# Kernel optimization log

Hardware: AMD Instinct MI355X
Metric: run time of the kernel (lower is better)

## Reference

```python
import jax, jax.numpy as jnp
import numpy as np

# Static config matching init_kwargs / forward constants
H = 12          # num_heads
D = 64          # head_dim
SW = 64         # kv_cache_sliding_window (frames)
SF = 8          # kv_cache_scale_frames
NUM_REG = 4     # num_register_tokens -> camera_idx=0, scale_idx=5
SPECIAL_END = NUM_REG + 2  # camera..scale inclusive slice = tokens [0:6)


def setup_inputs() -> dict:
    key = jax.random.key(0)
    ks = jax.random.split(key, 9)
    B, N, C = 1, 576, 768
    T = 192  # tokens per frame; num_frame_per_block = N // T = 3
    inp = {
        'x': jax.random.normal(ks[0], (B, N, C), jnp.float32),
        'qkv_w': jax.random.normal(ks[1], (3 * C, C), jnp.float32) * (C ** -0.5),
        'qkv_b': jax.random.normal(ks[2], (3 * C,), jnp.float32) * 0.02,
        'proj_w': jax.random.normal(ks[3], (C, C), jnp.float32) * (C ** -0.5),
        'proj_b': jax.random.normal(ks[4], (C,), jnp.float32) * 0.02,
        'k_cache': jax.random.normal(ks[5], (B, H, SW + SF, T, D), jnp.float32),
        'v_cache': jax.random.normal(ks[6], (B, H, SW + SF, T, D), jnp.float32),
        'k_special': jax.random.normal(ks[7], (B, H, 12, SPECIAL_END, D), jnp.float32),
        'v_special': jax.random.normal(ks[8], (B, H, 12, SPECIAL_END, D), jnp.float32),
    }
    return inp


def reference(x, qkv_w, qkv_b, proj_w, proj_b, k_cache, v_cache, k_special, v_special):
    B, N, C = x.shape
    T = k_cache.shape[3]           # tokens per frame
    nfb = N // T                   # num_frame_per_block (inferred, as in torch code)

    # qkv projection: (B,N,3C) -> (3,B,H,N,D)
    qkv = (x @ qkv_w.T + qkv_b).reshape(B, N, 3, H, D).transpose(2, 0, 3, 1, 4)
    q, k, v = qkv[0], qkv[1], qkv[2]   # each (B,H,N,D); q_norm/k_norm = Identity

    # Append new block frames to the cache
    k_cache = jnp.concatenate([k_cache, k.reshape(B, H, nfb, T, D)], axis=2)
    v_cache = jnp.concatenate([v_cache, v.reshape(B, H, nfb, T, D)], axis=2)

    # Sliding-window eviction (shapes chosen so this branch always fires)
    F = k_cache.shape[2]
    evict_start, evict_end = SF, F - SW   # 8 .. 11
    # cross-frame special tokens: camera..scale (tokens 0:6) of evicted frames
    new_sk = k_cache[:, :, evict_start:evict_end, :SPECIAL_END, :]
    new_sv = v_cache[:, :, evict_start:evict_end, :SPECIAL_END, :]
    k_special = jnp.concatenate([k_special, new_sk], axis=2)
    v_special = jnp.concatenate([v_special, new_sv], axis=2)
    # keep scale frames + last sliding_window frames
    k_cache = jnp.concatenate([k_cache[:, :, :SF], k_cache[:, :, -SW:]], axis=2)
    v_cache = jnp.concatenate([v_cache[:, :, :SF], v_cache[:, :, -SW:]], axis=2)

    # Flatten frames -> tokens; prepend special tokens
    k_full = jnp.concatenate([k_special.reshape(B, H, -1, D),
                              k_cache.reshape(B, H, -1, D)], axis=2)
    v_full = jnp.concatenate([v_special.reshape(B, H, -1, D),
                              v_cache.reshape(B, H, -1, D)], axis=2)

    # SDPA (no mask, no dropout, default scale 1/sqrt(D))
    scale = 1.0 / jnp.sqrt(jnp.float32(D))
    scores = jnp.einsum('bhnd,bhmd->bhnm', q, k_full) * scale
    attn = jax.nn.softmax(scores, axis=-1)
    out = jnp.einsum('bhnm,bhmd->bhnd', attn, v_full)

    out = out.transpose(0, 2, 1, 3).reshape(B, N, H * D)
    return out @ proj_w.T + proj_b
```

## Files before the change

kernel.cpp:

```cpp
#include <hip/hip_runtime.h>
#include <hip/hip_bf16.h>

#define NH    12
#define HD    64
#define NT    576
#define CC    768
#define M_TOT 13914
#define MP    13952
#define NTIL  218
#define NEW0  13338

typedef short bf16x8 __attribute__((ext_vector_type(8)));
typedef float f32x4 __attribute__((ext_vector_type(4)));
typedef float f32x16 __attribute__((ext_vector_type(16)));

#define QSCALE 0.18033688011112042f

__device__ __forceinline__ unsigned pk2(float a, float b) {
  __hip_bfloat162 h = __float22bfloat162_rn(make_float2(a, b));
  return *(unsigned*)&h;
}

__global__ __launch_bounds__(256) void cvt_all(
    const float* __restrict__ x, const float* __restrict__ wsrc,
    const float* __restrict__ pw, __hip_bfloat16* __restrict__ xb,
    __hip_bfloat16* __restrict__ wb, __hip_bfloat16* __restrict__ wph,
    __hip_bfloat16* __restrict__ wpl) {
  const int nx8 = NT * CC / 8;
  const int nw8 = 3 * CC * CC / 8;
  const int npw8 = CC * CC / 8;
  int i = blockIdx.x * 256 + threadIdx.x;
  if (i < nx8 + nw8) {
    const float* src; __hip_bfloat16* dst; int j;
    if (i < nx8) { src = x; dst = xb; j = i; }
    else { j = i - nx8; src = wsrc; dst = wb; }
    const float4 a = ((const float4*)src)[2 * j];
    const float4 b = ((const float4*)src)[2 * j + 1];
    __hip_bfloat16 t[8];
    t[0] = __float2bfloat16(a.x); t[1] = __float2bfloat16(a.y);
    t[2] = __float2bfloat16(a.z); t[3] = __float2bfloat16(a.w);
    t[4] = __float2bfloat16(b.x); t[5] = __float2bfloat16(b.y);
    t[6] = __float2bfloat16(b.z); t[7] = __float2bfloat16(b.w);
    ((uint4*)dst)[j] = *(const uint4*)t;
  } else {
    const int j = i - nx8 - nw8;
    if (j >= npw8) return;
    float v[8];
    const float4 a = ((const float4*)pw)[2 * j];
    const float4 b = ((const float4*)pw)[2 * j + 1];
    v[0] = a.x; v[1] = a.y; v[2] = a.z; v[3] = a.w;
    v[4] = b.x; v[5] = b.y; v[6] = b.z; v[7] = b.w;
    __hip_bfloat16 th[8], tl[8];
#pragma unroll
    for (int e = 0; e < 8; ++e) {
      th[e] = __float2bfloat16(v[e]);
      tl[e] = __float2bfloat16(v[e] - __bfloat162float(th[e]));
    }
    ((uint4*)wph)[j] = *(const uint4*)th;
    ((uint4*)wpl)[j] = *(const uint4*)tl;
  }
}

__device__ __forceinline__ const float* kv_src_row(
    const float* __restrict__ cache, const float* __restrict__ special,
    int h, int m) {
  if (m < 72) return special + ((size_t)h * 72 + m) * HD;
  if (m < 90) {
    const int j = m - 72;
    return cache + (((size_t)h * 72 + 8 + j / 6) * 192 + (j % 6)) * HD;
  }
  if (m < 1626) return cache + ((size_t)h * 13824 + (m - 90)) * HD;
  return cache + ((size_t)h * 13824 + 2112 + (m - 1626)) * HD;
}

#define GEMM_BLKS 324
#define VT_BLKS   2616
#define KB_BLKS   10004

__global__ __launch_bounds__(256) void qkv_and_gather(
    const __hip_bfloat16* __restrict__ xb, const __hip_bfloat16* __restrict__ wb,
    const float* __restrict__ bias, __hip_bfloat16* __restrict__ Qb,
    __hip_bfloat16* __restrict__ Kf, __hip_bfloat16* __restrict__ Vt,
    const float* __restrict__ kc, const float* __restrict__ ksp,
    const float* __restrict__ vc, const float* __restrict__ vsp) {
  __shared__ float vsf[64][68];
  const int bx = blockIdx.x;
  const int tid = threadIdx.x;

  if (bx < GEMM_BLKS) {
    const int w = tid >> 6, l = tid & 63, l15 = l & 15, lg = l >> 4;
    const int n0 = (bx % 36) * 64;
    const int mw = (bx / 36) * 64 + w * 16;

    f32x4 acc[4];
#pragma unroll
    for (int nt = 0; nt < 4; ++nt) acc[nt] = (f32x4){0.f, 0.f, 0.f, 0.f};

    const __hip_bfloat16* arow = xb + (size_t)(mw + l15) * CC + 8 * lg;
#pragma unroll 4
    for (int k0 = 0; k0 < CC; k0 += 32) {
      const bf16x8 a = *(const bf16x8*)(arow + k0);
#pragma unroll
      for (int nt = 0; nt < 4; ++nt) {
        const bf16x8 b =
            *(const bf16x8*)(wb + (size_t)(n0 + nt * 16 + l15) * CC + k0 + 8 * lg);
        acc[nt] = __builtin_amdgcn_mfma_f32_16x16x32_bf16(a, b, acc[nt], 0, 0, 0);
      }
    }
#pragma unroll
    for (int nt = 0; nt < 4; ++nt) {
      const int c = n0 + nt * 16 + l15;
      const int which = c / CC;
      const int rem = c - which * CC;
      const int hh = rem >> 6;
      const int dd = rem & 63;
      const float bc = bias[c];
#pragma unroll
      for (int r = 0; r < 4; ++r) {
        const int m = mw + 4 * lg + r;
        const float v = acc[nt][r] + bc;
        if (which == 0) {
          Qb[((size_t)hh * NT + m) * HD + dd] = __float2bfloat16(v * QSCALE);
        } else if (which == 1) {
          Kf[((size_t)hh * MP + NEW0 + m) * HD + dd] = __float2bfloat16(v);
        } else {
          Vt[((size_t)hh * HD + dd) * MP + NEW0 + m] = __float2bfloat16(v);
        }
      }
    }
  } else if (bx < GEMM_BLKS + VT_BLKS) {
    const int tv = bx - GEMM_BLKS;
    const int m0 = (tv % 218) * 64;
    const int h = tv / 218;
    if (m0 >= NEW0) return;
#pragma unroll
    for (int p = 0; p < 4; ++p) {
      const int mr = m0 + p * 16 + (tid >> 4);
      const int c4 = (tid & 15) * 4;
      float4 v = make_float4(0.f, 0.f, 0.f, 0.f);
      if (mr < NEW0) v = *(const float4*)(kv_src_row(vc, vsp, h, mr) + c4);
      *(float4*)&vsf[p * 16 + (tid >> 4)][c4] = v;
    }
    __syncthreads();
#pragma unroll
    for (int e0 = 0; e0 < 2; ++e0) {
      const int e = tid + e0 * 256;
      const int d = e >> 3;
      const int ms = (e & 7) * 8;
      __hip_bfloat16 t[8];
#pragma unroll
      for (int j = 0; j < 8; ++j) t[j] = __float2bfloat16(vsf[ms + j][d]);
      __hip_bfloat16* dst = Vt + ((size_t)h * HD + d) * MP + m0 + ms;
      if (m0 + ms + 8 <= NEW0) {
        *(uint4*)dst = *(const uint4*)t;
      } else {
#pragma unroll
        for (int j = 0; j < 8; ++j)
          if (m0 + ms + j < NEW0) dst[j] = t[j];
      }
    }
  } else {
    const int idx = (bx - GEMM_BLKS - VT_BLKS) * 256 + tid;
    const int per_h = NEW0 * 16;
    if (idx >= NH * per_h) return;
    const int h = idx / per_h;
    const int r = idx - h * per_h;
    const int m = r >> 4;
    const int dq = (r & 15) << 2;
    const float4 v = *(const float4*)(kv_src_row(kc, ksp, h, m) + dq);
    __hip_bfloat162* dst = (__hip_bfloat162*)(Kf + ((size_t)h * MP + m) * HD + dq);
    __hip_bfloat162 a, b;
    a.x = __float2bfloat16(v.x); a.y = __float2bfloat16(v.y);
    b.x = __float2bfloat16(v.z); b.y = __float2bfloat16(v.w);
    dst[0] = a; dst[1] = b;
  }
}

template <int S>
__global__ __launch_bounds__(256, 4) void attn_partial(
    const __hip_bfloat16* __restrict__ Qb, const __hip_bfloat16* __restrict__ Kf,
    const __hip_bfloat16* __restrict__ Vt, float* __restrict__ Opart,
    float2* __restrict__ mlpart) {
  __shared__ __align__(16) char lds[32768];

  const int tid = threadIdx.x;
  const int w = tid >> 6, l = tid & 63;
  const int l31 = l & 31, hi = l >> 5;

  const int i = blockIdx.x;
  const int per_xcd = (5 * NH * S) / 8;
  const int work = (i & 7) * per_xcd + (i >> 3);
  const int qt = work % 5;
  const int hs = work / 5;
  const int h = hs % NH;
  const int strip = hs / NH;

  const int qrow = qt * 128 + w * 32 + l31;
  const int qrc = qrow < NT ? qrow : NT - 1;

  bf16x8 qreg[4];
  {
    const __hip_bfloat16* qp = Qb + ((size_t)h * NT + qrc) * HD + 8 * hi;
#pragma unroll
    for (int s4 = 0; s4 < 4; ++s4) qreg[s4] = *(const bf16x8*)(qp + 16 * s4);
  }

  f32x16 oacc0, oacc1;
#pragma unroll
  for (int r = 0; r < 16; ++r) { oacc0[r] = 0.f; oacc1[r] = 0.f; }
  float m_run = -1e30f, l_run = 0.f;

  const __hip_bfloat16* Kh = Kf + (size_t)h * MP * HD;
  const __hip_bfloat16* Vth = Vt + (size_t)h * HD * MP;

  const int srow0 = tid >> 3;
  const int srow1 = 32 + (tid >> 3);
  const int sp8 = (tid & 7) * 8;
  const unsigned soff0 =
      ((unsigned)((srow0 << 7) | ((tid & 7) << 4))) ^ ((srow0 & 7) << 4);
  const unsigned soff1 =
      ((unsigned)((srow1 << 7) | ((tid & 7) << 4))) ^ ((srow1 & 7) << 4);

  uint4 kd0, kd1, vd0, vd1;
  auto issue = [&](int t) {
    const int m0 = t * 64;
    kd0 = *(const uint4*)(Kh + (size_t)(m0 + srow0) * HD + sp8);
    kd1 = *(const uint4*)(Kh + (size_t)(m0 + srow1) * HD + sp8);
    vd0 = *(const uint4*)(Vth + (size_t)srow0 * MP + m0 + sp8);
    vd1 = *(const uint4*)(Vth + (size_t)srow1 * MP + m0 + sp8);
  };
  auto commit = [&](char* buf) {
    *(uint4*)(buf + soff0) = kd0;
    *(uint4*)(buf + soff1) = kd1;
    *(uint4*)(buf + 8192 + soff0) = vd0;
    *(uint4*)(buf + 8192 + soff1) = vd1;
  };

  issue(strip);
  commit(lds);
  __syncthreads();

  int cur = 0;
  for (int t = strip; t < NTIL; t += S) {
    const int tn = t + S;
    if (tn < NTIL) issue(tn);

    char* ksb = lds + (cur << 14);
    char* vtb = ksb + 8192;
    const int m0 = t * 64;

    f32x16 sc0, sc1;
#pragma unroll
    for (int r = 0; r < 16; ++r) { sc0[r] = 0.f; sc1[r] = 0.f; }
#pragma unroll
    for (int s4 = 0; s4 < 4; ++s4) {
      const int cb = 32 * s4 + 16 * hi;
      const unsigned o0 = ((unsigned)((l31 << 7) | cb)) ^ ((l31 & 7) << 4);
      const unsigned o1 = ((unsigned)(((l31 + 32) << 7) | cb)) ^ ((l31 & 7) << 4);
      const bf16x8 a0 = *(const bf16x8*)(ksb + o0);
      const bf16x8 a1 = *(const bf16x8*)(ksb + o1);
      sc0 = __builtin_amdgcn_mfma_f32_32x32x16_bf16(a0, qreg[s4], sc0, 0, 0, 0);
      sc1 = __builtin_amdgcn_mfma_f32_32x32x16_bf16(a1, qreg[s4], sc1, 0, 0, 0);
    }

    if (m0 + 64 > M_TOT) {
#pragma unroll
      for (int r = 0; r < 16; ++r) {
        const int base = (r & 3) + 8 * (r >> 2) + 4 * hi;
        if (m0 + base >= M_TOT) sc0[r] = -1e30f;
        if (m0 + 32 + base >= M_TOT) sc1[r] = -1e30f;
      }
    }

    float mt = sc0[0];
#pragma unroll
    for (int r = 1; r < 16; ++r) mt = fmaxf(mt, sc0[r]);
#pragma unroll
    for (int r = 0; r < 16; ++r) mt = fmaxf(mt, sc1[r]);
    mt = fmaxf(mt, __shfl_xor(mt, 32));

    if (__any(mt > m_run + 8.f)) {
      const float mn = fmaxf(m_run, mt);
      const float corr = exp2f(m_run - mn);
      m_run = mn;
      l_run *= corr;
#pragma unroll
      for (int r = 0; r < 16; ++r) { oacc0[r] *= corr; oacc1[r] *= corr; }
    }

    float psum = 0.f;
    unsigned W0[8], W1[8];
#pragma unroll
    for (int i2 = 0; i2 < 8; ++i2) {
      const float e0 = exp2f(sc0[2 * i2] - m_run);
      const float e1 = exp2f(sc0[2 * i2 + 1] - m_run);
      const float f0 = exp2f(sc1[2 * i2] - m_run);
      const float f1 = exp2f(sc1[2 * i2 + 1] - m_run);
      psum += (e0 + e1) + (f0 + f1);
      W0[i2] = pk2(e0, e1);
      W1[i2] = pk2(f0, f1);
    }
    psum += __shfl_xor(psum, 32);
    l_run += psum;

#pragma unroll
    for (int s4 = 0; s4 < 4; ++s4) {
      const int u = s4 & 1;
      const unsigned a0 = (s4 < 2) ? W0[4 * u + 0] : W1[4 * u + 0];
      const unsigned a1 = (s4 < 2) ? W0[4 * u + 1] : W1[4 * u + 1];
      const unsigned a2 = (s4 < 2) ? W0[4 * u + 2] : W1[4 * u + 2];
      const unsigned a3 = (s4 < 2) ? W0[4 * u + 3] : W1[4 * u + 3];
      const unsigned x0 = (unsigned)__shfl_xor((int)a0, 32);
      const unsigned x1 = (unsigned)__shfl_xor((int)a1, 32);
      const unsigned x2 = (unsigned)__shfl_xor((int)a2, 32);
      const unsigned x3 = (unsigned)__shfl_xor((int)a3, 32);
      union { unsigned u4[4]; bf16x8 v; } pa;
      pa.u4[0] = hi ? x2 : a0;
      pa.u4[1] = hi ? x3 : a1;
      pa.u4[2] = hi ? a2 : x0;
      pa.u4[3] = hi ? a3 : x1;
      const int cb = 32 * s4 + 16 * hi;
#pragma unroll
      for (int dh = 0; dh < 2; ++dh) {
        const int vr = 32 * dh + l31;
        const unsigned ov = ((unsigned)((vr << 7) | cb)) ^ ((vr & 7) << 4);
        const bf16x8 va = *(const bf16x8*)(vtb + ov);
        if (dh == 0)
          oacc0 = __builtin_amdgcn_mfma_f32_32x32x16_bf16(va, pa.v, oacc0, 0, 0, 0);
        else
          oacc1 = __builtin_amdgcn_mfma_f32_32x32x16_bf16(va, pa.v, oacc1, 0, 0, 0);
      }
    }

    if (tn < NTIL) commit(lds + ((cur ^ 1) << 14));
    __syncthreads();
    cur ^= 1;
  }

  if (qrow < NT) {
    float* Op = Opart + (((size_t)strip * NH + h) * NT + qrow) * HD;
#pragma unroll
    for (int g = 0; g < 4; ++g) {
      f32x4 o0 = {oacc0[4 * g], oacc0[4 * g + 1], oacc0[4 * g + 2], oacc0[4 * g + 3]};
      f32x4 o1 = {oacc1[4 * g], oacc1[4 * g + 1], oacc1[4 * g + 2], oacc1[4 * g + 3]};
      *(f32x4*)(Op + 8 * g + 4 * hi) = o0;
      *(f32x4*)(Op + 32 + 8 * g + 4 * hi) = o1;
    }
    if (hi == 0)
      mlpart[((size_t)strip * NH + h) * NT + qrow] = make_float2(m_run, l_run);
  }
}

template <int S>
__global__ __launch_bounds__(256) void attn_merge(
    const float* __restrict__ Opart, const float2* __restrict__ mlpart,
    __hip_bfloat16* __restrict__ Owh, __hip_bfloat16* __restrict__ Owl) {
  const int idx = blockIdx.x * 256 + threadIdx.x;
  if (idx >= NH * NT * HD) return;
  const int d = idx & 63;
  const int hn = idx >> 6;
  const int n = hn % NT;
  const int h = hn / NT;
  float M = -1e30f;
  float m[S], lv[S];
#pragma unroll
  for (int s = 0; s < S; ++s) {
    const float2 ml = mlpart[((size_t)s * NH + h) * NT + n];
    m[s] = ml.x; lv[s] = ml.y;
    M = fmaxf(M, m[s]);
  }
  float L = 0.f, O = 0.f;
#pragma unroll
  for (int s = 0; s < S; ++s) {
    const float e = exp2f(m[s] - M);
    L += lv[s] * e;
    O += Opart[(((size_t)s * NH + h) * NT + n) * HD + d] * e;
  }
  const float v = O / L;
  const __hip_bfloat16 hB = __float2bfloat16(v);
  const size_t o = (size_t)n * CC + h * HD + d;
  Owh[o] = hB;
  Owl[o] = __float2bfloat16(v - __bfloat162float(hB));
}

__global__ __launch_bounds__(256) void gemm_proj_mfma(
    const __hip_bfloat16* __restrict__ Ah, const __hip_bfloat16* __restrict__ Al,
    const __hip_bfloat16* __restrict__ Wh, const __hip_bfloat16* __restrict__ Wl,
    const float* __restrict__ bias, float* __restrict__ out_f) {
  const int tid = threadIdx.x;
  const int w = tid >> 6, l = tid & 63, l15 = l & 15, lg = l >> 4;
  const int n0 = blockIdx.x * 64;
  const int mw = blockIdx.y * 64 + w * 16;

  f32x4 acc[4];
#pragma unroll
  for (int nt = 0; nt < 4; ++nt) acc[nt] = (f32x4){0.f, 0.f, 0.f, 0.f};

  const __hip_bfloat16* ah = Ah + (size_t)(mw + l15) * CC + 8 * lg;
  const __hip_bfloat16* al = Al + (size_t)(mw + l15) * CC + 8 * lg;
#pragma unroll 2
  for (int k0 = 0; k0 < CC; k0 += 32) {
    const bf16x8 a0 = *(const bf16x8*)(ah + k0);
    const bf16x8 a1 = *(const bf16x8*)(al + k0);
#pragma unroll
    for (int nt = 0; nt < 4; ++nt) {
      const size_t wi = (size_t)(n0 + nt * 16 + l15) * CC + k0 + 8 * lg;
      const bf16x8 bh = *(const bf16x8*)(Wh + wi);
      const bf16x8 bl = *(const bf16x8*)(Wl + wi);
      acc[nt] = __builtin_amdgcn_mfma_f32_16x16x32_bf16(a0, bh, acc[nt], 0, 0, 0);
      acc[nt] = __builtin_amdgcn_mfma_f32_16x16x32_bf16(a0, bl, acc[nt], 0, 0, 0);
      acc[nt] = __builtin_amdgcn_mfma_f32_16x16x32_bf16(a1, bh, acc[nt], 0, 0, 0);
    }
  }
#pragma unroll
  for (int nt = 0; nt < 4; ++nt) {
    const int c = n0 + nt * 16 + l15;
    const float bc = bias[c];
#pragma unroll
    for (int r = 0; r < 4; ++r)
      out_f[(size_t)(mw + 4 * lg + r) * CC + c] = acc[nt][r] + bc;
  }
}

extern "C" void kernel_launch(void* const* d_in, const int* in_sizes, int n_in,
                              void* d_out, int out_size, void* d_ws,
                              size_t ws_size, hipStream_t stream) {
  const float* x       = (const float*)d_in[0];
  const float* qkv_w   = (const float*)d_in[1];
  const float* qkv_b   = (const float*)d_in[2];
  const float* proj_w  = (const float*)d_in[3];
  const float* proj_b  = (const float*)d_in[4];
  const float* k_cache = (const float*)d_in[5];
  const float* v_cache = (const float*)d_in[6];
  const float* k_specl = (const float*)d_in[7];
  const float* v_specl = (const float*)d_in[8];
  float* out = (float*)d_out;

  const size_t qb_bytes = (size_t)NH * NT * HD * 2;
  const size_t kv_bytes = (size_t)NH * MP * HD * 2;
  const size_t xb_bytes = (size_t)NT * CC * 2;
  const size_t wb_bytes = (size_t)3 * CC * CC * 2;
  const size_t pw_bytes = (size_t)CC * CC * 2;
  const size_t owh_bytes = (size_t)NT * CC * 2;

  auto need = [&](int S) -> size_t {
    const size_t op = (size_t)S * NH * NT * HD * 4;
    const size_t ml = (size_t)S * NH * NT * 8;
    const size_t opr = op > xb_bytes + wb_bytes ? op : xb_bytes + wb_bytes;
    return qb_bytes + 2 * kv_bytes + opr + ml + 2 * pw_bytes;
  };
  const int S = (need(16) <= ws_size) ? 16 : 8;
  const size_t op_bytes = (size_t)S * NH * NT * HD * 4;
  const size_t ml_bytes = (size_t)S * NH * NT * 8;
  const size_t opr = op_bytes > xb_bytes + wb_bytes ? op_bytes : xb_bytes + wb_bytes;

  char* ws = (char*)d_ws;
  __hip_bfloat16* Qb = (__hip_bfloat16*)ws;
  char* kf_region = ws + qb_bytes;
  __hip_bfloat16* Kf = (__hip_bfloat16*)kf_region;
  __hip_bfloat16* Vt = (__hip_bfloat16*)(kf_region + kv_bytes);
  char* opp = kf_region + 2 * kv_bytes;
  float* Opart = (float*)opp;
  __hip_bfloat16* xb = (__hip_bfloat16*)opp;
  __hip_bfloat16* wb = (__hip_bfloat16*)(opp + xb_bytes);
  float2* mlpart = (float2*)(opp + opr);
  __hip_bfloat16* wph = (__hip_bfloat16*)(opp + opr + ml_bytes);
  __hip_bfloat16* wpl = (__hip_bfloat16*)(opp + opr + ml_bytes + pw_bytes);
  __hip_bfloat16* Owh = (__hip_bfloat16*)kf_region;
  __hip_bfloat16* Owl = (__hip_bfloat16*)(kf_region + owh_bytes);

  cvt_all<<<dim3(1368), 256, 0, stream>>>(x, qkv_w, proj_w, xb, wb, wph, wpl);
  qkv_and_gather<<<dim3(GEMM_BLKS + VT_BLKS + KB_BLKS), 256, 0, stream>>>(
      xb, wb, qkv_b, Qb, Kf, Vt, k_cache, k_specl, v_cache, v_specl);
  if (S == 16) {
    attn_partial<16><<<dim3(5 * NH * 16), 256, 0, stream>>>(Qb, Kf, Vt, Opart, mlpart);
    attn_merge<16><<<dim3((NH * NT * HD + 255) / 256), 256, 0, stream>>>(
        Opart, mlpart, Owh, Owl);
  } else {
    attn_partial<8><<<dim3(5 * NH * 8), 256, 0, stream>>>(Qb, Kf, Vt, Opart, mlpart);
    attn_merge<8><<<dim3((NH * NT * HD + 255) / 256), 256, 0, stream>>>(
        Opart, mlpart, Owh, Owl);
  }
  gemm_proj_mfma<<<dim3(12, 9), 256, 0, stream>>>(Owh, Owl, wph, wpl, proj_b, out);
}
```

Baseline: 141.4 us.

## Fuse K-cache fp32-to-bf16 gather into attention kernel, drop double buffering

Removes the separate K gather and convert pass from the qkv kernel. The attention kernel now reads fp32 K rows straight from the cache and special-token buffers, converts them to bf16 in registers, and writes them into LDS. This avoids writing and re-reading a bf16 K copy, but each K tile is now read as fp32 by every query tile (5 times). The register-prefetch double buffer is replaced by a single-buffered load-sync-compute loop, and the projection GEMM uses 32-wide N tiles to launch twice as many blocks.

```diff
diff --git a/kernel.cpp b/kernel.cpp
--- a/kernel.cpp
+++ b/kernel.cpp
@@ -75,13 +75,11 @@
 
 #define GEMM_BLKS 324
 #define VT_BLKS   2616
-#define KB_BLKS   10004
 
 __global__ __launch_bounds__(256) void qkv_and_gather(
     const __hip_bfloat16* __restrict__ xb, const __hip_bfloat16* __restrict__ wb,
     const float* __restrict__ bias, __hip_bfloat16* __restrict__ Qb,
     __hip_bfloat16* __restrict__ Kf, __hip_bfloat16* __restrict__ Vt,
-    const float* __restrict__ kc, const float* __restrict__ ksp,
     const float* __restrict__ vc, const float* __restrict__ vsp) {
   __shared__ float vsf[64][68];
   const int bx = blockIdx.x;
@@ -128,7 +126,7 @@
         }
       }
     }
-  } else if (bx < GEMM_BLKS + VT_BLKS) {
+  } else {
     const int tv = bx - GEMM_BLKS;
     const int m0 = (tv % 218) * 64;
     const int h = tv / 218;
@@ -159,29 +157,18 @@
           if (m0 + ms + j < NEW0) dst[j] = t[j];
       }
     }
-  } else {
-    const int idx = (bx - GEMM_BLKS - VT_BLKS) * 256 + tid;
-    const int per_h = NEW0 * 16;
-    if (idx >= NH * per_h) return;
-    const int h = idx / per_h;
-    const int r = idx - h * per_h;
-    const int m = r >> 4;
-    const int dq = (r & 15) << 2;
-    const float4 v = *(const float4*)(kv_src_row(kc, ksp, h, m) + dq);
-    __hip_bfloat162* dst = (__hip_bfloat162*)(Kf + ((size_t)h * MP + m) * HD + dq);
-    __hip_bfloat162 a, b;
-    a.x = __float2bfloat16(v.x); a.y = __float2bfloat16(v.y);
-    b.x = __float2bfloat16(v.z); b.y = __float2bfloat16(v.w);
-    dst[0] = a; dst[1] = b;
   }
 }
 
 template <int S>
 __global__ __launch_bounds__(256, 4) void attn_partial(
     const __hip_bfloat16* __restrict__ Qb, const __hip_bfloat16* __restrict__ Kf,
-    const __hip_bfloat16* __restrict__ Vt, float* __restrict__ Opart,
+    const __hip_bfloat16* __restrict__ Vt, const float* __restrict__ kc,
+    const float* __restrict__ ksp, float* __restrict__ Opart,
     float2* __restrict__ mlpart) {
-  __shared__ __align__(16) char lds[32768];
+  __shared__ __align__(16) char lds[16384];
+  char* ksb = lds;
+  char* vtb = lds + 8192;
 
   const int tid = threadIdx.x;
   const int w = tid >> 6, l = tid & 63;
@@ -221,33 +208,28 @@
   const unsigned soff1 =
       ((unsigned)((srow1 << 7) | ((tid & 7) << 4))) ^ ((srow1 & 7) << 4);
 
-  uint4 kd0, kd1, vd0, vd1;
-  auto issue = [&](int t) {
+  for (int t = strip; t < NTIL; t += S) {
     const int m0 = t * 64;
-    kd0 = *(const uint4*)(Kh + (size_t)(m0 + srow0) * HD + sp8);
-    kd1 = *(const uint4*)(Kh + (size_t)(m0 + srow1) * HD + sp8);
-    vd0 = *(const uint4*)(Vth + (size_t)srow0 * MP + m0 + sp8);
-    vd1 = *(const uint4*)(Vth + (size_t)srow1 * MP + m0 + sp8);
-  };
-  auto commit = [&](char* buf) {
-    *(uint4*)(buf + soff0) = kd0;
-    *(uint4*)(buf + soff1) = kd1;
-    *(uint4*)(buf + 8192 + soff0) = vd0;
-    *(uint4*)(buf + 8192 + soff1) = vd1;
-  };
-
-  issue(strip);
-  commit(lds);
-  __syncthreads();
-
-  int cur = 0;
-  for (int t = strip; t < NTIL; t += S) {
-    const int tn = t + S;
-    if (tn < NTIL) issue(tn);
-
-    char* ksb = lds + (cur << 14);
-    char* vtb = ksb + 8192;
-    const int m0 = t * 64;
+#pragma unroll
+    for (int e = 0; e < 4; ++e) {
+      const int c = tid + 256 * e;
+      const int row = c >> 4, ci = c & 15;
+      const int m = m0 + row;
+      const unsigned off =
+          ((unsigned)((row << 7) | (ci << 3))) ^ ((unsigned)(row & 7) << 4);
+      uint2 w8;
+      if (m < NEW0) {
+        const float4 v = *(const float4*)(kv_src_row(kc, ksp, h, m) + 4 * ci);
+        w8.x = pk2(v.x, v.y);
+        w8.y = pk2(v.z, v.w);
+      } else {
+        w8 = *(const uint2*)(Kh + (size_t)m * HD + 4 * ci);
+      }
+      *(uint2*)(ksb + off) = w8;
+    }
+    *(uint4*)(vtb + soff0) = *(const uint4*)(Vth + (size_t)srow0 * MP + m0 + sp8);
+    *(uint4*)(vtb + soff1) = *(const uint4*)(Vth + (size_t)srow1 * MP + m0 + sp8);
+    __syncthreads();
 
     f32x16 sc0, sc1;
 #pragma unroll
@@ -331,10 +313,7 @@
           oacc1 = __builtin_amdgcn_mfma_f32_32x32x16_bf16(va, pa.v, oacc1, 0, 0, 0);
       }
     }
-
-    if (tn < NTIL) commit(lds + ((cur ^ 1) << 14));
     __syncthreads();
-    cur ^= 1;
   }
 
   if (qrow < NT) {
@@ -389,12 +368,12 @@
     const float* __restrict__ bias, float* __restrict__ out_f) {
   const int tid = threadIdx.x;
   const int w = tid >> 6, l = tid & 63, l15 = l & 15, lg = l >> 4;
-  const int n0 = blockIdx.x * 64;
+  const int n0 = blockIdx.x * 32;
   const int mw = blockIdx.y * 64 + w * 16;
 
-  f32x4 acc[4];
-#pragma unroll
-  for (int nt = 0; nt < 4; ++nt) acc[nt] = (f32x4){0.f, 0.f, 0.f, 0.f};
+  f32x4 acc[2];
+#pragma unroll
+  for (int nt = 0; nt < 2; ++nt) acc[nt] = (f32x4){0.f, 0.f, 0.f, 0.f};
 
   const __hip_bfloat16* ah = Ah + (size_t)(mw + l15) * CC + 8 * lg;
   const __hip_bfloat16* al = Al + (size_t)(mw + l15) * CC + 8 * lg;
@@ -403,7 +382,7 @@
     const bf16x8 a0 = *(const bf16x8*)(ah + k0);
     const bf16x8 a1 = *(const bf16x8*)(al + k0);
 #pragma unroll
-    for (int nt = 0; nt < 4; ++nt) {
+    for (int nt = 0; nt < 2; ++nt) {
       const size_t wi = (size_t)(n0 + nt * 16 + l15) * CC + k0 + 8 * lg;
       const bf16x8 bh = *(const bf16x8*)(Wh + wi);
       const bf16x8 bl = *(const bf16x8*)(Wl + wi);
@@ -413,7 +392,7 @@
     }
   }
 #pragma unroll
-  for (int nt = 0; nt < 4; ++nt) {
+  for (int nt = 0; nt < 2; ++nt) {
     const int c = n0 + nt * 16 + l15;
     const float bc = bias[c];
 #pragma unroll
@@ -470,16 +449,18 @@
   __hip_bfloat16* Owl = (__hip_bfloat16*)(kf_region + owh_bytes);
 
   cvt_all<<<dim3(1368), 256, 0, stream>>>(x, qkv_w, proj_w, xb, wb, wph, wpl);
-  qkv_and_gather<<<dim3(GEMM_BLKS + VT_BLKS + KB_BLKS), 256, 0, stream>>>(
-      xb, wb, qkv_b, Qb, Kf, Vt, k_cache, k_specl, v_cache, v_specl);
+  qkv_and_gather<<<dim3(GEMM_BLKS + VT_BLKS), 256, 0, stream>>>(
+      xb, wb, qkv_b, Qb, Kf, Vt, v_cache, v_specl);
   if (S == 16) {
-    attn_partial<16><<<dim3(5 * NH * 16), 256, 0, stream>>>(Qb, Kf, Vt, Opart, mlpart);
+    attn_partial<16><<<dim3(5 * NH * 16), 256, 0, stream>>>(
+        Qb, Kf, Vt, k_cache, k_specl, Opart, mlpart);
     attn_merge<16><<<dim3((NH * NT * HD + 255) / 256), 256, 0, stream>>>(
         Opart, mlpart, Owh, Owl);
   } else {
-    attn_partial<8><<<dim3(5 * NH * 8), 256, 0, stream>>>(Qb, Kf, Vt, Opart, mlpart);
+    attn_partial<8><<<dim3(5 * NH * 8), 256, 0, stream>>>(
+        Qb, Kf, Vt, k_cache, k_specl, Opart, mlpart);
     attn_merge<8><<<dim3((NH * NT * HD + 255) / 256), 256, 0, stream>>>(
         Opart, mlpart, Owh, Owl);
   }
-  gemm_proj_mfma<<<dim3(12, 9), 256, 0, stream>>>(Owh, Owl, wph, wpl, proj_b, out);
-}
+  gemm_proj_mfma<<<dim3(24, 9), 256, 0, stream>>>(Owh, Owl, wph, wpl, proj_b, out);
+}
```

Result: no change. 141.7 us (+0.2%).

## Drop attention LDS double-buffering and halve projection GEMM tile width

Applied to the files above, without the earlier changes.

The attention kernel's register-staged double-buffered K/V prefetch is replaced by a single 16KB LDS buffer, loaded synchronously at the top of each tile iteration. This halves LDS use and frees the prefetch registers, which may allow more resident blocks, but global load latency is no longer hidden behind MFMA work. Separately, the projection GEMM tile is narrowed from 64 to 32 output columns and the grid is doubled, giving more blocks for better CU coverage at the cost of more redundant A-row loads.

```diff
diff --git a/kernel.cpp b/kernel.cpp
--- a/kernel.cpp
+++ b/kernel.cpp
@@ -181,7 +181,9 @@
     const __hip_bfloat16* __restrict__ Qb, const __hip_bfloat16* __restrict__ Kf,
     const __hip_bfloat16* __restrict__ Vt, float* __restrict__ Opart,
     float2* __restrict__ mlpart) {
-  __shared__ __align__(16) char lds[32768];
+  __shared__ __align__(16) char lds[16384];
+  char* ksb = lds;
+  char* vtb = lds + 8192;
 
   const int tid = threadIdx.x;
   const int w = tid >> 6, l = tid & 63;
@@ -213,41 +215,19 @@
   const __hip_bfloat16* Kh = Kf + (size_t)h * MP * HD;
   const __hip_bfloat16* Vth = Vt + (size_t)h * HD * MP;
 
-  const int srow0 = tid >> 3;
-  const int srow1 = 32 + (tid >> 3);
-  const int sp8 = (tid & 7) * 8;
-  const unsigned soff0 =
-      ((unsigned)((srow0 << 7) | ((tid & 7) << 4))) ^ ((srow0 & 7) << 4);
-  const unsigned soff1 =
-      ((unsigned)((srow1 << 7) | ((tid & 7) << 4))) ^ ((srow1 & 7) << 4);
-
-  uint4 kd0, kd1, vd0, vd1;
-  auto issue = [&](int t) {
+  for (int t = strip; t < NTIL; t += S) {
     const int m0 = t * 64;
-    kd0 = *(const uint4*)(Kh + (size_t)(m0 + srow0) * HD + sp8);
-    kd1 = *(const uint4*)(Kh + (size_t)(m0 + srow1) * HD + sp8);
-    vd0 = *(const uint4*)(Vth + (size_t)srow0 * MP + m0 + sp8);
-    vd1 = *(const uint4*)(Vth + (size_t)srow1 * MP + m0 + sp8);
-  };
-  auto commit = [&](char* buf) {
-    *(uint4*)(buf + soff0) = kd0;
-    *(uint4*)(buf + soff1) = kd1;
-    *(uint4*)(buf + 8192 + soff0) = vd0;
-    *(uint4*)(buf + 8192 + soff1) = vd1;
-  };
-
-  issue(strip);
-  commit(lds);
-  __syncthreads();
-
-  int cur = 0;
-  for (int t = strip; t < NTIL; t += S) {
-    const int tn = t + S;
-    if (tn < NTIL) issue(tn);
-
-    char* ksb = lds + (cur << 14);
-    char* vtb = ksb + 8192;
-    const int m0 = t * 64;
+#pragma unroll
+    for (int e = 0; e < 2; ++e) {
+      const int c = tid + 256 * e;
+      const int row = c >> 3, p = c & 7;
+      const unsigned off = ((unsigned)((row << 7) | (p << 4))) ^ ((row & 7) << 4);
+      const uint4 kd = *(const uint4*)(Kh + (size_t)(m0 + row) * HD + p * 8);
+      const uint4 vd = *(const uint4*)(Vth + (size_t)row * MP + m0 + p * 8);
+      *(uint4*)(ksb + off) = kd;
+      *(uint4*)(vtb + off) = vd;
+    }
+    __syncthreads();
 
     f32x16 sc0, sc1;
 #pragma unroll
@@ -331,10 +311,7 @@
           oacc1 = __builtin_amdgcn_mfma_f32_32x32x16_bf16(va, pa.v, oacc1, 0, 0, 0);
       }
     }
-
-    if (tn < NTIL) commit(lds + ((cur ^ 1) << 14));
     __syncthreads();
-    cur ^= 1;
   }
 
   if (qrow < NT) {
@@ -389,12 +366,12 @@
     const float* __restrict__ bias, float* __restrict__ out_f) {
   const int tid = threadIdx.x;
   const int w = tid >> 6, l = tid & 63, l15 = l & 15, lg = l >> 4;
-  const int n0 = blockIdx.x * 64;
+  const int n0 = blockIdx.x * 32;
   const int mw = blockIdx.y * 64 + w * 16;
 
-  f32x4 acc[4];
-#pragma unroll
-  for (int nt = 0; nt < 4; ++nt) acc[nt] = (f32x4){0.f, 0.f, 0.f, 0.f};
+  f32x4 acc[2];
+#pragma unroll
+  for (int nt = 0; nt < 2; ++nt) acc[nt] = (f32x4){0.f, 0.f, 0.f, 0.f};
 
   const __hip_bfloat16* ah = Ah + (size_t)(mw + l15) * CC + 8 * lg;
   const __hip_bfloat16* al = Al + (size_t)(mw + l15) * CC + 8 * lg;
@@ -403,7 +380,7 @@
     const bf16x8 a0 = *(const bf16x8*)(ah + k0);
     const bf16x8 a1 = *(const bf16x8*)(al + k0);
 #pragma unroll
-    for (int nt = 0; nt < 4; ++nt) {
+    for (int nt = 0; nt < 2; ++nt) {
       const size_t wi = (size_t)(n0 + nt * 16 + l15) * CC + k0 + 8 * lg;
       const bf16x8 bh = *(const bf16x8*)(Wh + wi);
       const bf16x8 bl = *(const bf16x8*)(Wl + wi);
@@ -413,7 +390,7 @@
     }
   }
 #pragma unroll
-  for (int nt = 0; nt < 4; ++nt) {
+  for (int nt = 0; nt < 2; ++nt) {
     const int c = n0 + nt * 16 + l15;
     const float bc = bias[c];
 #pragma unroll
@@ -481,5 +458,5 @@
     attn_merge<8><<<dim3((NH * NT * HD + 255) / 256), 256, 0, stream>>>(
         Opart, mlpart, Owh, Owl);
   }
-  gemm_proj_mfma<<<dim3(12, 9), 256, 0, stream>>>(Owh, Owl, wph, wpl, proj_b, out);
-}
+  gemm_proj_mfma<<<dim3(24, 9), 256, 0, stream>>>(Owh, Owl, wph, wpl, proj_b, out);
+}
```

Result: faster. 127.4 us (-9.9%).
